# Performance work log

Hardware: AMD Instinct MI355X
Metric: run time of the kernel (lower is better)

## Reference

```python
import jax, jax.numpy as jnp
import numpy as np

N_NODES = 100000
N_EDGES = 1600000
D_IN = 128
D_HID = 128
D_OUT = 128


def setup_inputs() -> dict:
    key = jax.random.key(0)
    ks = jax.random.split(key, 9)
    x = jax.random.normal(ks[0], (N_NODES, D_IN), dtype=jnp.float32)
    src = jax.random.randint(ks[1], (N_EDGES,), 0, N_NODES, dtype=jnp.int32)
    dst = jax.random.randint(ks[2], (N_EDGES,), 0, N_NODES, dtype=jnp.int32)
    s = 1.0 / np.sqrt(D_IN)
    Wc = jax.random.uniform(ks[3], (D_IN, D_HID), dtype=jnp.float32, minval=-s, maxval=s)
    bc = jnp.zeros((D_HID,), dtype=jnp.float32)
    s1 = 1.0 / np.sqrt(D_HID)
    W1 = jax.random.uniform(ks[4], (D_HID, D_HID), dtype=jnp.float32, minval=-s1, maxval=s1)
    b1 = jax.random.uniform(ks[5], (D_HID,), dtype=jnp.float32, minval=-s1, maxval=s1)
    W2 = jax.random.uniform(ks[6], (D_HID, D_OUT), dtype=jnp.float32, minval=-s1, maxval=s1)
    b2 = jax.random.uniform(ks[7], (D_OUT,), dtype=jnp.float32, minval=-s1, maxval=s1)
    return {"x": x, "src": src, "dst": dst, "Wc": Wc, "bc": bc,
            "W1": W1, "b1": b1, "W2": W2, "b2": b2}


def reference(x, src, dst, Wc, bc, W1, b1, W2, b2):
    # DGL GraphConv with norm='both' (default), no edge_weight:
    #   h = x / sqrt(out_deg(src));  agg[v] = sum_{(u->v)} h[u];  agg /= sqrt(in_deg(v))
    ones = jnp.ones((src.shape[0],), dtype=x.dtype)
    deg_out = jax.ops.segment_sum(ones, src, num_segments=N_NODES)
    deg_in = jax.ops.segment_sum(ones, dst, num_segments=N_NODES)
    norm_out = jax.lax.rsqrt(jnp.clip(deg_out, 1.0))[:, None]  # [N,1]
    norm_in = jax.lax.rsqrt(jnp.clip(deg_in, 1.0))[:, None]

    h = x * norm_out
    msgs = h[src]                                              # [E, D_in]
    agg = jax.ops.segment_sum(msgs, dst, num_segments=N_NODES) # [N, D_in]
    agg = agg * norm_in
    h = agg @ Wc + bc                                          # GraphConv linear

    # num_layers == 2 path: relu -> fc -> relu -> fc2
    h = jax.nn.relu(h)
    h = h @ W1 + b1
    h = jax.nn.relu(h)
    out = h @ W2 + b2
    return out
```

## Files before the change

kernel.cpp:

```cpp
#include <hip/hip_runtime.h>
#include <hip/hip_fp16.h>

#define NN 100000
#define NE 1600000
#define NBK 782
#define MAXB 2560
#define EPB 4096
#define NPB 391

typedef __attribute__((ext_vector_type(8))) __bf16 bf16x8;
typedef __attribute__((ext_vector_type(4))) float f32x4;

__global__ __launch_bounds__(256) void initcur_kernel(int* __restrict__ cursorA,
                                                      int* __restrict__ cursorO) {
    int b = blockIdx.x * 256 + threadIdx.x;
    if (b < NBK) { cursorA[b] = b * MAXB; cursorO[b] = b * MAXB; }
}

__global__ __launch_bounds__(256) void phase1_kernel(const int* __restrict__ src,
                                                     const int* __restrict__ dst,
                                                     int* __restrict__ cursorA,
                                                     int* __restrict__ cursorO,
                                                     int* __restrict__ tempA,
                                                     unsigned char* __restrict__ tempO8) {
    __shared__ int cntA[NBK], cntO[NBK];
    const int t = threadIdx.x;
    for (int b = t; b < NBK; b += 256) { cntA[b] = 0; cntO[b] = 0; }
    __syncthreads();
    const int e0 = blockIdx.x * EPB;
    int rD[16], rS[16];
#pragma unroll
    for (int i = 0; i < 16; ++i) {
        int e = e0 + i * 256 + t;
        if (e < NE) {
            rD[i] = atomicAdd(&cntA[dst[e] >> 7], 1);
            rS[i] = atomicAdd(&cntO[src[e] >> 7], 1);
        }
    }
    __syncthreads();
    for (int b = t; b < NBK; b += 256) {
        int c = cntA[b];
        cntA[b] = c ? atomicAdd(&cursorA[b], c) : 0;
        c = cntO[b];
        cntO[b] = c ? atomicAdd(&cursorO[b], c) : 0;
    }
    __syncthreads();
#pragma unroll
    for (int i = 0; i < 16; ++i) {
        int e = e0 + i * 256 + t;
        if (e < NE) {
            int d = dst[e], s = src[e];
            tempA[cntA[d >> 7] + rD[i]] = ((d & 127) << 17) | s;
            tempO8[cntO[s >> 7] + rS[i]] = (unsigned char)(s & 127);
        }
    }
}

__global__ __launch_bounds__(1024) void bscan_kernel(const int* __restrict__ cursorA,
                                                     int* __restrict__ edgeBase) {
    __shared__ int sm[1024];
    int t = threadIdx.x;
    int v = (t < NBK) ? (cursorA[t] - t * MAXB) : 0;
    sm[t] = v;
    __syncthreads();
    for (int o = 1; o < 1024; o <<= 1) {
        int u = (t >= o) ? sm[t - o] : 0;
        __syncthreads();
        sm[t] += u;
        __syncthreads();
    }
    if (t < NBK) edgeBase[t] = sm[t] - v;
}

__global__ __launch_bounds__(256) void phase2_kernel(const int* __restrict__ cursorA,
                                                     const int* __restrict__ cursorO,
                                                     const int* __restrict__ tempA,
                                                     const unsigned char* __restrict__ tempO8,
                                                     const int* __restrict__ edgeBase,
                                                     const float* __restrict__ x,
                                                     int* __restrict__ csr_src,
                                                     int* __restrict__ rowptr,
                                                     float* __restrict__ normI,
                                                     __half* __restrict__ xh) {
    __shared__ int buf[MAXB];
    __shared__ int cnt[128], ex[128], run[128], cntO[128];
    const int b = blockIdx.x;
    const int t = threadIdx.x;
    const int cA = cursorA[b] - b * MAXB;
    const int cO = cursorO[b] - b * MAXB;
    const int base = edgeBase[b];
    if (t < 128) { cnt[t] = 0; cntO[t] = 0; run[t] = 0; }
    __syncthreads();
    for (int i = t; i < cA; i += 256) {
        int w = tempA[b * MAXB + i];
        buf[i] = w;
        atomicAdd(&cnt[(w >> 17) & 127], 1);
    }
    for (int i = t; i < cO; i += 256)
        atomicAdd(&cntO[tempO8[b * MAXB + i]], 1);
    __syncthreads();
    {
        int r = t >> 1;
        int node = b * 128 + r;
        if (node < NN) {
            float nO = rsqrtf(fmaxf((float)cntO[r], 1.0f));
            int c0 = (t & 1) * 64;
#pragma unroll
            for (int i = 0; i < 16; ++i) {
                float4 v = *reinterpret_cast<const float4*>(&x[(size_t)node * 128 + c0 + i * 4]);
                __half2 h01 = __floats2half2_rn(v.x * nO, v.y * nO);
                __half2 h23 = __floats2half2_rn(v.z * nO, v.w * nO);
                __half2 hh[2] = {h01, h23};
                *reinterpret_cast<float2*>(&xh[(size_t)node * 128 + c0 + i * 4]) =
                    *reinterpret_cast<float2*>(hh);
            }
        }
    }
    if (t < 128) ex[t] = cnt[t];
    __syncthreads();
    for (int o = 1; o < 128; o <<= 1) {
        int u = (t >= o && t < 128) ? ex[t - o] : 0;
        __syncthreads();
        if (t < 128) ex[t] += u;
        __syncthreads();
    }
    if (t < 128) {
        int node = b * 128 + t;
        if (node < NN) {
            rowptr[node] = base + ex[t] - cnt[t];
            normI[node] = rsqrtf(fmaxf((float)cnt[t], 1.0f));
        }
    }
    if (b == 0 && t == 0) rowptr[NN] = NE;
    __syncthreads();
    for (int i = t; i < cA; i += 256) {
        int w = buf[i];
        int n = (w >> 17) & 127;
        int r = atomicAdd(&run[n], 1);
        csr_src[base + ex[n] - cnt[n] + r] = w & 0x1FFFF;
    }
}

__global__ __launch_bounds__(256) void gather_kernel(const __half* __restrict__ xh,
                                                     const int* __restrict__ rowptr,
                                                     const int* __restrict__ csr_src,
                                                     const float* __restrict__ normI,
                                                     float* __restrict__ agg) {
    int node = blockIdx.x * 8 + (threadIdx.x >> 5);
    int lane = threadIdx.x & 31;
    if (node >= NN) return;
    int beg = rowptr[node], end = rowptr[node + 1];
    float ax = 0.f, ay = 0.f, az = 0.f, aw = 0.f;
    int j = beg;
    for (; j + 4 <= end; j += 4) {
        int s0 = csr_src[j], s1 = csr_src[j + 1], s2 = csr_src[j + 2], s3 = csr_src[j + 3];
        float2 r0 = *reinterpret_cast<const float2*>(&xh[(size_t)s0 * 128 + lane * 4]);
        float2 r1 = *reinterpret_cast<const float2*>(&xh[(size_t)s1 * 128 + lane * 4]);
        float2 r2 = *reinterpret_cast<const float2*>(&xh[(size_t)s2 * 128 + lane * 4]);
        float2 r3 = *reinterpret_cast<const float2*>(&xh[(size_t)s3 * 128 + lane * 4]);
        const __half2* p0 = reinterpret_cast<const __half2*>(&r0);
        const __half2* p1 = reinterpret_cast<const __half2*>(&r1);
        const __half2* p2 = reinterpret_cast<const __half2*>(&r2);
        const __half2* p3 = reinterpret_cast<const __half2*>(&r3);
        float2 l0 = __half22float2(p0[0]), h0 = __half22float2(p0[1]);
        float2 l1 = __half22float2(p1[0]), h1 = __half22float2(p1[1]);
        float2 l2 = __half22float2(p2[0]), h2 = __half22float2(p2[1]);
        float2 l3 = __half22float2(p3[0]), h3 = __half22float2(p3[1]);
        ax += l0.x + l1.x + l2.x + l3.x;
        ay += l0.y + l1.y + l2.y + l3.y;
        az += h0.x + h1.x + h2.x + h3.x;
        aw += h0.y + h1.y + h2.y + h3.y;
    }
    for (; j < end; ++j) {
        int s = csr_src[j];
        float2 r = *reinterpret_cast<const float2*>(&xh[(size_t)s * 128 + lane * 4]);
        const __half2* p = reinterpret_cast<const __half2*>(&r);
        float2 l = __half22float2(p[0]), h = __half22float2(p[1]);
        ax += l.x; ay += l.y; az += h.x; aw += h.y;
    }
    float ni = normI[node];
    float4 o = make_float4(ax * ni, ay * ni, az * ni, aw * ni);
    *reinterpret_cast<float4*>(&agg[(size_t)node * 128 + lane * 4]) = o;
}

__global__ __launch_bounds__(256) void wprep_kernel(const float* __restrict__ Wc,
                                                    const float* __restrict__ W1,
                                                    const float* __restrict__ W2,
                                                    __bf16* __restrict__ Wf) {
    int t = blockIdx.x * 256 + threadIdx.x;
    if (t >= 3 * 4 * 8 * 64) return;
    int lane = t & 63;
    int ct = (t >> 6) & 7;
    int kt = (t >> 9) & 3;
    int layer = t >> 11;
    const float* W = (layer == 0) ? Wc : (layer == 1) ? W1 : W2;
    int c = ct * 16 + (lane & 15);
    int kbase = kt * 32 + (lane >> 4) * 8;
    bf16x8 hi, lo;
#pragma unroll
    for (int j = 0; j < 8; ++j) {
        float wv = W[(size_t)(kbase + j) * 128 + c];
        __bf16 h = (__bf16)wv;
        hi[j] = h;
        lo[j] = (__bf16)(wv - (float)h);
    }
    bf16x8* Wv = reinterpret_cast<bf16x8*>(Wf);
    Wv[((size_t)((layer * 2 + 0) * 4 + kt) * 8 + ct) * 64 + lane] = hi;
    Wv[((size_t)((layer * 2 + 1) * 4 + kt) * 8 + ct) * 64 + lane] = lo;
}

__global__ __launch_bounds__(256, 2) void mlp_mfma(const float* __restrict__ A,
                                                   const __bf16* __restrict__ Wf,
                                                   const float* __restrict__ bc,
                                                   const float* __restrict__ b1,
                                                   const float* __restrict__ b2,
                                                   float* __restrict__ C, int n) {
    __shared__ float HS[64][132];
    __shared__ char WL[2][16384];
    const int tid = threadIdx.x;
    const int lane = tid & 63;
    const int wv = tid >> 6;
    const int row0 = blockIdx.x * 64;
    const int mrow = lane & 15;
    const int kg = lane >> 4;
    const char* Wb = (const char*)Wf;

#pragma unroll
    for (int i = 0; i < 4; ++i) {
        const int c = i * 4 + wv;
        const int h = c >> 3, ct7 = c & 7;
        size_t goff = ((size_t)((h * 4 + 0) * 8 + ct7)) * 1024 + (size_t)lane * 16;
        __builtin_amdgcn_global_load_lds(
            (const __attribute__((address_space(1))) unsigned int*)(Wb + goff),
            (__attribute__((address_space(3))) unsigned int*)(&WL[0][c * 1024 + lane * 16]),
            16, 0, 0);
    }

    {
        int r = tid >> 5;
        int c4 = (tid & 31) * 4;
#pragma unroll
        for (int i = 0; i < 8; ++i) {
            int row = i * 8 + r;
            int grow = row0 + row;
            float4 v = make_float4(0.f, 0.f, 0.f, 0.f);
            if (grow < n)
                v = *reinterpret_cast<const float4*>(&A[(size_t)grow * 128 + c4]);
            *reinterpret_cast<float4*>(&HS[row][c4]) = v;
        }
    }
    float bv[3][8];
#pragma unroll
    for (int ct = 0; ct < 8; ++ct) {
        bv[0][ct] = bc[ct * 16 + mrow];
        bv[1][ct] = b1[ct * 16 + mrow];
        bv[2][ct] = b2[ct * 16 + mrow];
    }
    __syncthreads();

    f32x4 acc[8];
#pragma unroll
    for (int s = 0; s < 12; ++s) {
        const int layer = s >> 2, kt = s & 3, buf = s & 1;
        if (kt == 0) {
#pragma unroll
            for (int ct = 0; ct < 8; ++ct) acc[ct] = (f32x4){0.f, 0.f, 0.f, 0.f};
        }
        if (s > 0) {
            asm volatile("s_waitcnt vmcnt(0)" ::: "memory");
            __builtin_amdgcn_s_barrier();
        }
        if (s < 11) {
            const int s1 = s + 1;
            const int ly = s1 >> 2, k2 = s1 & 3, bf = s1 & 1;
#pragma unroll
            for (int i = 0; i < 4; ++i) {
                const int c = i * 4 + wv;
                const int h = c >> 3, ct7 = c & 7;
                size_t goff = ((size_t)(((ly * 2 + h) * 4 + k2) * 8 + ct7)) * 1024 + (size_t)lane * 16;
                __builtin_amdgcn_global_load_lds(
                    (const __attribute__((address_space(1))) unsigned int*)(Wb + goff),
                    (__attribute__((address_space(3))) unsigned int*)(&WL[bf][c * 1024 + lane * 16]),
                    16, 0, 0);
            }
        }
        const bf16x8* WB = reinterpret_cast<const bf16x8*>(&WL[buf][0]);
        bf16x8 bhi[8], blo[8];
#pragma unroll
        for (int ct = 0; ct < 8; ++ct) {
            bhi[ct] = WB[ct * 64 + lane];
            blo[ct] = WB[512 + ct * 64 + lane];
        }
        const float* hsrc = &HS[wv * 16 + mrow][kt * 32 + kg * 8];
        float4 p0 = *reinterpret_cast<const float4*>(hsrc);
        float4 p1 = *reinterpret_cast<const float4*>(hsrc + 4);
        float av[8] = {p0.x, p0.y, p0.z, p0.w, p1.x, p1.y, p1.z, p1.w};
        bf16x8 ahi, alo;
#pragma unroll
        for (int j = 0; j < 8; ++j) {
            __bf16 h = (__bf16)av[j];
            ahi[j] = h;
            alo[j] = (__bf16)(av[j] - (float)h);
        }
#pragma unroll
        for (int ct = 0; ct < 8; ++ct) {
            acc[ct] = __builtin_amdgcn_mfma_f32_16x16x32_bf16(alo, bhi[ct], acc[ct], 0, 0, 0);
            acc[ct] = __builtin_amdgcn_mfma_f32_16x16x32_bf16(ahi, blo[ct], acc[ct], 0, 0, 0);
            acc[ct] = __builtin_amdgcn_mfma_f32_16x16x32_bf16(ahi, bhi[ct], acc[ct], 0, 0, 0);
        }
        if (kt == 3) {
            if (layer < 2) {
#pragma unroll
                for (int ct = 0; ct < 8; ++ct)
#pragma unroll
                    for (int r = 0; r < 4; ++r)
                        HS[wv * 16 + kg * 4 + r][ct * 16 + mrow] =
                            fmaxf(acc[ct][r] + bv[layer][ct], 0.f);
                asm volatile("s_waitcnt lgkmcnt(0)" ::: "memory");
            } else {
#pragma unroll
                for (int ct = 0; ct < 8; ++ct)
#pragma unroll
                    for (int r = 0; r < 4; ++r) {
                        int grow = row0 + wv * 16 + kg * 4 + r;
                        if (grow < n)
                            C[(size_t)grow * 128 + ct * 16 + mrow] = acc[ct][r] + bv[2][ct];
                    }
            }
        }
    }
}

extern "C" void kernel_launch(void* const* d_in, const int* in_sizes, int n_in,
                              void* d_out, int out_size, void* d_ws, size_t ws_size,
                              hipStream_t stream) {
    const float* x  = (const float*)d_in[0];
    const int*  src = (const int*)d_in[1];
    const int*  dst = (const int*)d_in[2];
    const float* Wc = (const float*)d_in[3];
    const float* bc = (const float*)d_in[4];
    const float* W1 = (const float*)d_in[5];
    const float* b1 = (const float*)d_in[6];
    const float* W2 = (const float*)d_in[7];
    const float* b2 = (const float*)d_in[8];
    float* out = (float*)d_out;

    char* p = (char*)d_ws;
    __bf16* Wf = (__bf16*)p;            p += 196608;
    __half* xh = (__half*)p;            p += (size_t)NN * 128 * 2;
    int* tempA = (int*)p;               p += (size_t)NBK * MAXB * 4;
    unsigned char* tempO8 = (unsigned char*)p; p += (size_t)NBK * MAXB;
    int* cursorA  = (int*)p;            p += (size_t)NBK * 4;
    int* cursorO  = (int*)p;            p += (size_t)NBK * 4;
    int* edgeBase = (int*)p;            p += (size_t)NBK * 4;
    int* rowptr   = (int*)p;            p += (size_t)(NN + 1) * 4;
    float* normI  = (float*)p;          p += (size_t)NN * 4;
    int* csr_src  = (int*)p;

    wprep_kernel<<<24, 256, 0, stream>>>(Wc, W1, W2, Wf);
    initcur_kernel<<<(NBK + 255) / 256, 256, 0, stream>>>(cursorA, cursorO);
    phase1_kernel<<<NPB, 256, 0, stream>>>(src, dst, cursorA, cursorO, tempA, tempO8);
    bscan_kernel<<<1, 1024, 0, stream>>>(cursorA, edgeBase);
    phase2_kernel<<<NBK, 256, 0, stream>>>(cursorA, cursorO, tempA, tempO8, edgeBase,
                                           x, csr_src, rowptr, normI, xh);

    gather_kernel<<<(NN + 7) / 8, 256, 0, stream>>>(xh, rowptr, csr_src, normI, out);

    mlp_mfma<<<(NN + 63) / 64, 256, 0, stream>>>(out, Wf, bc, b1, b2, out, NN);
}
```

Before: 214.5 us.

## Split MLP MFMA work by output columns per wave and pre-split activations to bf16 hi/lo

```diff
diff --git a/kernel.cpp b/kernel.cpp
--- a/kernel.cpp
+++ b/kernel.cpp
@@ -215,8 +215,8 @@
                                                    const float* __restrict__ b1,
                                                    const float* __restrict__ b2,
                                                    float* __restrict__ C, int n) {
-    __shared__ float HS[64][132];
-    __shared__ char WL[2][16384];
+    __shared__ unsigned HS2[64][132];
+    __shared__ char WB[4][2][4096];
     const int tid = threadIdx.x;
     const int lane = tid & 63;
     const int wv = tid >> 6;
@@ -226,13 +226,12 @@
     const char* Wb = (const char*)Wf;
 
 #pragma unroll
-    for (int i = 0; i < 4; ++i) {
-        const int c = i * 4 + wv;
-        const int h = c >> 3, ct7 = c & 7;
-        size_t goff = ((size_t)((h * 4 + 0) * 8 + ct7)) * 1024 + (size_t)lane * 16;
+    for (int sg = 0; sg < 4; ++sg) {
+        int h = sg >> 1, ctl = 2 * wv + (sg & 1);
+        size_t goff = ((size_t)((h * 4 + 0) * 8 + ctl)) * 1024 + (size_t)lane * 16;
         __builtin_amdgcn_global_load_lds(
             (const __attribute__((address_space(1))) unsigned int*)(Wb + goff),
-            (__attribute__((address_space(3))) unsigned int*)(&WL[0][c * 1024 + lane * 16]),
+            (__attribute__((address_space(3))) unsigned int*)(&WB[wv][0][sg * 1024]),
             16, 0, 0);
     }
 
@@ -246,86 +245,119 @@
             float4 v = make_float4(0.f, 0.f, 0.f, 0.f);
             if (grow < n)
                 v = *reinterpret_cast<const float4*>(&A[(size_t)grow * 128 + c4]);
-            *reinterpret_cast<float4*>(&HS[row][c4]) = v;
-        }
-    }
-    float bv[3][8];
-#pragma unroll
-    for (int ct = 0; ct < 8; ++ct) {
-        bv[0][ct] = bc[ct * 16 + mrow];
-        bv[1][ct] = b1[ct * 16 + mrow];
-        bv[2][ct] = b2[ct * 16 + mrow];
-    }
-    __syncthreads();
-
-    f32x4 acc[8];
+            float vv[4] = {v.x, v.y, v.z, v.w};
+            unsigned uu[4];
+#pragma unroll
+            for (int q = 0; q < 4; ++q) {
+                __bf16 h = (__bf16)vv[q];
+                unsigned short hb = __builtin_bit_cast(unsigned short, h);
+                __bf16 l = (__bf16)(vv[q] - (float)h);
+                unsigned short lb = __builtin_bit_cast(unsigned short, l);
+                uu[q] = (unsigned)hb | ((unsigned)lb << 16);
+            }
+            *reinterpret_cast<uint4*>(&HS2[row][c4]) = (uint4){uu[0], uu[1], uu[2], uu[3]};
+        }
+    }
+    float bvl[3][2];
+#pragma unroll
+    for (int c = 0; c < 2; ++c) {
+        int col = (2 * wv + c) * 16 + mrow;
+        bvl[0][c] = bc[col];
+        bvl[1][c] = b1[col];
+        bvl[2][c] = b2[col];
+    }
+    __syncthreads();
+
+    f32x4 acc[4][2];
+#pragma unroll
+    for (int m = 0; m < 4; ++m)
+#pragma unroll
+        for (int c = 0; c < 2; ++c) acc[m][c] = (f32x4){0.f, 0.f, 0.f, 0.f};
+
 #pragma unroll
     for (int s = 0; s < 12; ++s) {
         const int layer = s >> 2, kt = s & 3, buf = s & 1;
-        if (kt == 0) {
-#pragma unroll
-            for (int ct = 0; ct < 8; ++ct) acc[ct] = (f32x4){0.f, 0.f, 0.f, 0.f};
-        }
-        if (s > 0) {
-            asm volatile("s_waitcnt vmcnt(0)" ::: "memory");
-            __builtin_amdgcn_s_barrier();
-        }
         if (s < 11) {
             const int s1 = s + 1;
-            const int ly = s1 >> 2, k2 = s1 & 3, bf = s1 & 1;
-#pragma unroll
-            for (int i = 0; i < 4; ++i) {
-                const int c = i * 4 + wv;
-                const int h = c >> 3, ct7 = c & 7;
-                size_t goff = ((size_t)(((ly * 2 + h) * 4 + k2) * 8 + ct7)) * 1024 + (size_t)lane * 16;
+            const int l1 = s1 >> 2, k1 = s1 & 3, b1i = s1 & 1;
+#pragma unroll
+            for (int sg = 0; sg < 4; ++sg) {
+                int h = sg >> 1, ctl = 2 * wv + (sg & 1);
+                size_t goff = ((size_t)(((l1 * 2 + h) * 4 + k1) * 8 + ctl)) * 1024
+                            + (size_t)lane * 16;
                 __builtin_amdgcn_global_load_lds(
                     (const __attribute__((address_space(1))) unsigned int*)(Wb + goff),
-                    (__attribute__((address_space(3))) unsigned int*)(&WL[bf][c * 1024 + lane * 16]),
+                    (__attribute__((address_space(3))) unsigned int*)(&WB[wv][b1i][sg * 1024]),
                     16, 0, 0);
             }
-        }
-        const bf16x8* WB = reinterpret_cast<const bf16x8*>(&WL[buf][0]);
-        bf16x8 bhi[8], blo[8];
-#pragma unroll
-        for (int ct = 0; ct < 8; ++ct) {
-            bhi[ct] = WB[ct * 64 + lane];
-            blo[ct] = WB[512 + ct * 64 + lane];
-        }
-        const float* hsrc = &HS[wv * 16 + mrow][kt * 32 + kg * 8];
-        float4 p0 = *reinterpret_cast<const float4*>(hsrc);
-        float4 p1 = *reinterpret_cast<const float4*>(hsrc + 4);
-        float av[8] = {p0.x, p0.y, p0.z, p0.w, p1.x, p1.y, p1.z, p1.w};
-        bf16x8 ahi, alo;
-#pragma unroll
-        for (int j = 0; j < 8; ++j) {
-            __bf16 h = (__bf16)av[j];
-            ahi[j] = h;
-            alo[j] = (__bf16)(av[j] - (float)h);
-        }
-#pragma unroll
-        for (int ct = 0; ct < 8; ++ct) {
-            acc[ct] = __builtin_amdgcn_mfma_f32_16x16x32_bf16(alo, bhi[ct], acc[ct], 0, 0, 0);
-            acc[ct] = __builtin_amdgcn_mfma_f32_16x16x32_bf16(ahi, blo[ct], acc[ct], 0, 0, 0);
-            acc[ct] = __builtin_amdgcn_mfma_f32_16x16x32_bf16(ahi, bhi[ct], acc[ct], 0, 0, 0);
-        }
+            asm volatile("s_waitcnt vmcnt(4)" ::: "memory");
+        } else {
+            asm volatile("s_waitcnt vmcnt(0)" ::: "memory");
+        }
+
+        const char* wbase = &WB[wv][buf][0];
+        bf16x8 bhi[2], blo[2];
+#pragma unroll
+        for (int c = 0; c < 2; ++c) {
+            bhi[c] = *reinterpret_cast<const bf16x8*>(wbase + c * 1024 + lane * 16);
+            blo[c] = *reinterpret_cast<const bf16x8*>(wbase + (2 + c) * 1024 + lane * 16);
+        }
+#pragma unroll
+        for (int m = 0; m < 4; ++m) {
+            const unsigned* ap = &HS2[m * 16 + mrow][kt * 32 + kg * 8];
+            uint4 u0 = *reinterpret_cast<const uint4*>(ap);
+            uint4 u1 = *reinterpret_cast<const uint4*>(ap + 4);
+            unsigned uu[8] = {u0.x, u0.y, u0.z, u0.w, u1.x, u1.y, u1.z, u1.w};
+            unsigned hd[4], ld[4];
+#pragma unroll
+            for (int d = 0; d < 4; ++d) {
+                hd[d] = (uu[2 * d] & 0xFFFFu) | (uu[2 * d + 1] << 16);
+                ld[d] = (uu[2 * d] >> 16) | (uu[2 * d + 1] & 0xFFFF0000u);
+            }
+            bf16x8 ahi = __builtin_bit_cast(bf16x8, (uint4){hd[0], hd[1], hd[2], hd[3]});
+            bf16x8 alo = __builtin_bit_cast(bf16x8, (uint4){ld[0], ld[1], ld[2], ld[3]});
+#pragma unroll
+            for (int c = 0; c < 2; ++c) {
+                acc[m][c] = __builtin_amdgcn_mfma_f32_16x16x32_bf16(alo, bhi[c], acc[m][c], 0, 0, 0);
+                acc[m][c] = __builtin_amdgcn_mfma_f32_16x16x32_bf16(ahi, blo[c], acc[m][c], 0, 0, 0);
+                acc[m][c] = __builtin_amdgcn_mfma_f32_16x16x32_bf16(ahi, bhi[c], acc[m][c], 0, 0, 0);
+            }
+        }
+
         if (kt == 3) {
             if (layer < 2) {
-#pragma unroll
-                for (int ct = 0; ct < 8; ++ct)
-#pragma unroll
-                    for (int r = 0; r < 4; ++r)
-                        HS[wv * 16 + kg * 4 + r][ct * 16 + mrow] =
-                            fmaxf(acc[ct][r] + bv[layer][ct], 0.f);
+                asm volatile("s_barrier" ::: "memory");
+#pragma unroll
+                for (int m = 0; m < 4; ++m)
+#pragma unroll
+                    for (int c = 0; c < 2; ++c) {
+                        float bvv = bvl[layer][c];
+#pragma unroll
+                        for (int r = 0; r < 4; ++r) {
+                            float o = fmaxf(acc[m][c][r] + bvv, 0.f);
+                            __bf16 hh = (__bf16)o;
+                            unsigned short hb = __builtin_bit_cast(unsigned short, hh);
+                            __bf16 ll = (__bf16)(o - (float)hh);
+                            unsigned short lb = __builtin_bit_cast(unsigned short, ll);
+                            HS2[m * 16 + kg * 4 + r][(2 * wv + c) * 16 + mrow] =
+                                (unsigned)hb | ((unsigned)lb << 16);
+                            acc[m][c][r] = 0.f;
+                        }
+                    }
                 asm volatile("s_waitcnt lgkmcnt(0)" ::: "memory");
+                asm volatile("s_barrier" ::: "memory");
             } else {
 #pragma unroll
-                for (int ct = 0; ct < 8; ++ct)
-#pragma unroll
-                    for (int r = 0; r < 4; ++r) {
-                        int grow = row0 + wv * 16 + kg * 4 + r;
-                        if (grow < n)
-                            C[(size_t)grow * 128 + ct * 16 + mrow] = acc[ct][r] + bv[2][ct];
-                    }
+                for (int m = 0; m < 4; ++m)
+#pragma unroll
+                    for (int c = 0; c < 2; ++c)
+#pragma unroll
+                        for (int r = 0; r < 4; ++r) {
+                            int grow = row0 + m * 16 + kg * 4 + r;
+                            if (grow < n)
+                                C[(size_t)grow * 128 + (2 * wv + c) * 16 + mrow] =
+                                    acc[m][c][r] + bvl[2][c];
+                        }
             }
         }
     }
```

Result: no change. 211.2 us (-1.6%).
